# Optimization experiments

Hardware: AMD Instinct MI355X
Metric: run time of the kernel (lower is better)

Reference implementation:

```python
import jax, jax.numpy as jnp
import numpy as np

N, L, V, D, E, NL = 50000, 32, 5000, 128, 800000, 3
P, B = 5000, 64

def setup_inputs() -> dict:
    key = jax.random.key(0)
    ks = jax.random.split(key, 6)
    x = jax.random.randint(ks[0], (N, L), 0, V)            # token ids, 0 = pad
    edge_index = jax.random.randint(ks[1], (2, E), 0, N)   # [2,E] src,dst
    pool_idx = jnp.arange(N) // (N // P)                   # node -> pooled supernode
    node_batch = pool_idx * B // P                         # node -> graph id (grouped, as in torch loop)
    embed = jax.random.normal(ks[2], (V, D), jnp.float32) * 0.02
    W_l = jax.random.normal(ks[3], (NL, D, D), jnp.float32) / np.sqrt(D)
    W_r = jax.random.normal(ks[4], (NL, D, D), jnp.float32) / np.sqrt(D)
    b = jnp.zeros((NL, D), jnp.float32)
    return dict(x=x, edge_index=edge_index, pool_idx=pool_idx, node_batch=node_batch,
                num_pooled=P, embed=embed, W_l=W_l, W_r=W_r, b=b)

def reference(x, edge_index, pool_idx, node_batch, num_pooled, embed, W_l, W_r, b):
    n = x.shape[0]
    dt = embed.dtype
    # masked mean-pool of token embeddings (pad id = 0), length clamped to >=1
    mask = (x != 0)
    lengths = jnp.clip(mask.sum(axis=1), 1, None).astype(dt)          # [N]
    h = (embed[x] * mask[..., None].astype(dt)).sum(axis=1) / lengths[:, None]  # [N,D]
    src, dst = edge_index[0], edge_index[1]
    deg = jnp.clip(jax.ops.segment_sum(jnp.ones(src.shape[0], dt), dst, num_segments=n), 1.0, None)
    # SAGEConv layers: mean-aggregate neighbors, lin_l(agg)+bias + lin_r(self), relu
    # (dropout p=0.5 is identity in eval mode)
    for i in range(W_l.shape[0]):
        agg = jax.ops.segment_sum(h[src], dst, num_segments=n) / deg[:, None]
        h = jax.nn.relu(agg @ W_l[i] + b[i] + h @ W_r[i])
    # global mean pool over supernodes
    cnt = jnp.clip(jax.ops.segment_sum(jnp.ones(n, dt), pool_idx, num_segments=num_pooled), 1.0, None)
    x_pooled = jax.ops.segment_sum(h, pool_idx, num_segments=num_pooled) / cnt[:, None]
    # global max pool of graph ids -> pooled batch vector
    batch_pooled = jax.ops.segment_max(node_batch, pool_idx, num_segments=num_pooled)
    # coalesced pooled edges without self-loops, as a dense boolean adjacency
    sp, dp = pool_idx[src], pool_idx[dst]
    adj = jnp.zeros((num_pooled, num_pooled), jnp.bool_).at[sp, dp].set(True)
    adj = adj & ~jnp.eye(num_pooled, dtype=jnp.bool_)
    return x_pooled, adj, batch_pooled
```

## Files before the change

### kernel.cpp

```cpp
#include <hip/hip_runtime.h>
#include <hip/hip_fp16.h>
#include <limits.h>

#define D 128
#define SCL 64.0f

typedef __attribute__((ext_vector_type(8))) short bf16x8;
typedef __attribute__((ext_vector_type(4))) float f32x4;
typedef __attribute__((ext_vector_type(2))) float f32x2;

#if __has_builtin(__builtin_amdgcn_cvt_pk_f32_fp8) && __has_builtin(__builtin_amdgcn_cvt_pk_fp8_f32)
#define HW_FP8 1
#endif

static __device__ __forceinline__ unsigned short f2bf(float f) {
    unsigned u = __builtin_bit_cast(unsigned, f);
    u += 0x7FFFu + ((u >> 16) & 1u);
    return (unsigned short)(u >> 16);
}
static __device__ __forceinline__ float bf2f(unsigned u16) {
    unsigned u = u16 << 16;
    return __builtin_bit_cast(float, u);
}
static __device__ __forceinline__ bf16x8 load_frag(const unsigned short* p) {
    uint4 v = *(const uint4*)p;
    return __builtin_bit_cast(bf16x8, v);
}
static __device__ __forceinline__ ushort4 pack4(const float* a, float s) {
    ushort4 o;
    o.x = f2bf(a[0] * s); o.y = f2bf(a[1] * s);
    o.z = f2bf(a[2] * s); o.w = f2bf(a[3] * s);
    return o;
}

static __device__ __forceinline__ unsigned char f2q(float v) {
#ifdef HW_FP8
    return (unsigned char)(__builtin_amdgcn_cvt_pk_fp8_f32(v, v, 0, false) & 0xff);
#else
    unsigned short u = __half_as_ushort(__float2half(v));
    u = (unsigned short)(u + 0x7F + ((u >> 8) & 1));
    return (unsigned char)(u >> 8);
#endif
}
static __device__ __forceinline__ unsigned enc4(float a0, float a1, float a2, float a3) {
#ifdef HW_FP8
    unsigned u = __builtin_amdgcn_cvt_pk_fp8_f32(a0, a1, 0, false);
    u = __builtin_amdgcn_cvt_pk_fp8_f32(a2, a3, (int)u, true);
    return u;
#else
    return (unsigned)f2q(a0) | ((unsigned)f2q(a1) << 8) |
           ((unsigned)f2q(a2) << 16) | ((unsigned)f2q(a3) << 24);
#endif
}
static __device__ __forceinline__ void dec4(float* a, unsigned u) {
#ifdef HW_FP8
    f32x2 lo = __builtin_amdgcn_cvt_pk_f32_fp8((int)u, false);
    f32x2 hi = __builtin_amdgcn_cvt_pk_f32_fp8((int)u, true);
    a[0] += lo.x; a[1] += lo.y; a[2] += hi.x; a[3] += hi.y;
#else
    a[0] += __half2float(__ushort_as_half((unsigned short)((u & 0xff) << 8)));
    a[1] += __half2float(__ushort_as_half((unsigned short)(((u >> 8) & 0xff) << 8)));
    a[2] += __half2float(__ushort_as_half((unsigned short)(((u >> 16) & 0xff) << 8)));
    a[3] += __half2float(__ushort_as_half((unsigned short)((u >> 24) << 8)));
#endif
}

__global__ __launch_bounds__(256) void zero_k(float4* __restrict__ b, size_t nb)
{
    size_t i = (size_t)blockIdx.x * 256 + threadIdx.x;
    if (i < nb) b[i] = make_float4(0.f, 0.f, 0.f, 0.f);
}

__global__ __launch_bounds__(256) void epack_k(
    const float* __restrict__ embed, unsigned* __restrict__ e8, int n4)
{
    int i = blockIdx.x * 256 + threadIdx.x;
    if (i >= n4) return;
    float4 v = *(const float4*)&embed[(size_t)i * 4];
    e8[i] = enc4(v.x * SCL, v.y * SCL, v.z * SCL, v.w * SCL);
}

__global__ __launch_bounds__(256) void wpack_k(
    const float* __restrict__ Wl, const float* __restrict__ Wr,
    unsigned short* __restrict__ Wp, int NL)
{
    int idx = blockIdx.x * 256 + threadIdx.x;
    if (idx >= NL * 2 * 16384) return;
    int m = idx >> 14;
    int r = idx & 16383;
    int j = r & 7;
    int lane = (r >> 3) & 63;
    int cb = (r >> 9) & 7;
    int kb = (r >> 12) & 3;
    const float* W = ((m & 1) ? Wr : Wl) + (size_t)(m >> 1) * D * D;
    int k = kb * 32 + (lane >> 4) * 8 + j;
    int c = cb * 16 + (lane & 15);
    Wp[idx] = f2bf(W[(size_t)k * D + c]);
}

__global__ __launch_bounds__(256) void embed_pool_k(
    const int* __restrict__ x, const unsigned char* __restrict__ e8,
    unsigned short* __restrict__ h16, unsigned char* __restrict__ h8, int n, int L)
{
    __shared__ int toks[16][32];
    int t = threadIdx.x;
    int sub = t >> 4, s = t & 15;
    int node = blockIdx.x * 16 + sub;
    for (int j = t; j < 16 * L; j += 256) {
        int nd = blockIdx.x * 16 + j / L;
        toks[j / L][j % L] = (nd < n) ? x[(size_t)nd * L + (j % L)] : 0;
    }
    __syncthreads();
    if (node >= n) return;
    float acc[8] = {};
    int cnt = 0;
    for (int l = 0; l < L; ++l) {
        int tok = toks[sub][l];
        if (tok != 0) {
            uint2 v = *(const uint2*)&e8[(size_t)tok * D + s * 8];
            dec4(acc, v.x); dec4(acc + 4, v.y);
            cnt++;
        }
    }
    float c = (float)(cnt > 0 ? cnt : 1);
    float invh = 1.0f / (SCL * c);
    float inv8 = 1.0f / c;
    ushort4 lo = pack4(acc, invh), hi = pack4(acc + 4, invh);
    *(ushort4*)&h16[(size_t)node * D + s * 8]     = lo;
    *(ushort4*)&h16[(size_t)node * D + s * 8 + 4] = hi;
    uint2 q;
    q.x = enc4(acc[0] * inv8, acc[1] * inv8, acc[2] * inv8, acc[3] * inv8);
    q.y = enc4(acc[4] * inv8, acc[5] * inv8, acc[6] * inv8, acc[7] * inv8);
    *(uint2*)&h8[(size_t)node * D + s * 8] = q;
}

__global__ __launch_bounds__(256) void deg_k(
    const int* __restrict__ ei, int* __restrict__ deg, int E)
{
    int e = blockIdx.x * 256 + threadIdx.x;
    if (e >= E) return;
    atomicAdd(&deg[ei[E + e]], 1);
}

__global__ __launch_bounds__(256) void scan_partial_k(
    const int* __restrict__ deg, int* __restrict__ bsum, int n)
{
    int b = blockIdx.x, t = threadIdx.x;
    int i0 = b * 1024 + t * 4;
    int s = 0;
    #pragma unroll
    for (int k = 0; k < 4; ++k) { int i = i0 + k; if (i < n) s += deg[i]; }
    for (int off = 32; off > 0; off >>= 1) s += __shfl_down(s, off, 64);
    __shared__ int sm4[4];
    if ((t & 63) == 0) sm4[t >> 6] = s;
    __syncthreads();
    if (t == 0) bsum[b] = sm4[0] + sm4[1] + sm4[2] + sm4[3];
}

__global__ __launch_bounds__(256) void scan_bsum_k(
    const int* __restrict__ bsum, int* __restrict__ boff, int nb)
{
    __shared__ int sm[256];
    int t = threadIdx.x;
    sm[t] = (t < nb) ? bsum[t] : 0;
    __syncthreads();
    for (int off = 1; off < 256; off <<= 1) {
        int add = (t >= off) ? sm[t - off] : 0;
        __syncthreads();
        sm[t] += add;
        __syncthreads();
    }
    if (t < nb) boff[t] = (t > 0) ? sm[t - 1] : 0;
}

__global__ __launch_bounds__(256) void scan_final_k(
    const int* __restrict__ deg, const int* __restrict__ boff,
    int* __restrict__ rp, int n)
{
    __shared__ int sm[256];
    int b = blockIdx.x, t = threadIdx.x;
    int i0 = b * 1024 + t * 4;
    int v[4];
    #pragma unroll
    for (int k = 0; k < 4; ++k) { int i = i0 + k; v[k] = (i < n) ? deg[i] : 0; }
    v[1] += v[0]; v[2] += v[1]; v[3] += v[2];
    sm[t] = v[3];
    __syncthreads();
    for (int off = 1; off < 256; off <<= 1) {
        int add = (t >= off) ? sm[t - off] : 0;
        __syncthreads();
        sm[t] += add;
        __syncthreads();
    }
    int base = boff[b] + ((t > 0) ? sm[t - 1] : 0);
    if (b == 0 && t == 0) rp[0] = 0;
    #pragma unroll
    for (int k = 0; k < 4; ++k) {
        int i = i0 + k;
        if (i < n) rp[i + 1] = base + v[k];
    }
}

__global__ __launch_bounds__(256) void edge_pass2_k(
    const int* __restrict__ ei, const int* __restrict__ rp,
    const int* __restrict__ pool, int* __restrict__ cur,
    int* __restrict__ col, float* __restrict__ adj, int E, int P)
{
    int e = blockIdx.x * 256 + threadIdx.x;
    if (e >= E) return;
    int src = ei[e], dst = ei[E + e];
    int pos = atomicAdd(&cur[dst], 1);
    col[rp[dst] + pos] = src;
    int sp = pool[src], dp = pool[dst];
    if (sp != dp) adj[(size_t)sp * P + dp] = 1.0f;
}

__global__ __launch_bounds__(256) void aggregate_k(
    const unsigned char* __restrict__ h8, const int* __restrict__ rp,
    const int* __restrict__ col, unsigned short* __restrict__ agg16, int n)
{
    int node = blockIdx.x * 4 + (threadIdx.x >> 6);
    int lane = threadIdx.x & 63;
    if (node >= n) return;
    int beg = rp[node], end = rp[node + 1];
    int q = lane >> 4, s = lane & 15;
    float acc[8] = {};
    int e = beg + q;
    for (; e + 4 < end; e += 8) {
        int c0 = col[e], c1 = col[e + 4];
        uint2 v0 = *(const uint2*)&h8[(size_t)c0 * D + s * 8];
        uint2 v1 = *(const uint2*)&h8[(size_t)c1 * D + s * 8];
        dec4(acc, v0.x); dec4(acc + 4, v0.y);
        dec4(acc, v1.x); dec4(acc + 4, v1.y);
    }
    if (e < end) {
        uint2 v0 = *(const uint2*)&h8[(size_t)col[e] * D + s * 8];
        dec4(acc, v0.x); dec4(acc + 4, v0.y);
    }
    #pragma unroll
    for (int k = 0; k < 8; ++k) {
        acc[k] += __shfl_xor(acc[k], 16, 64);
        acc[k] += __shfl_xor(acc[k], 32, 64);
    }
    if (q == 0) {
        int dg = end - beg;
        float inv = 1.0f / (SCL * (float)(dg > 0 ? dg : 1));
        ushort4 lo = pack4(acc, inv), hi = pack4(acc + 4, inv);
        *(ushort4*)&agg16[(size_t)node * D + s * 8]     = lo;
        *(ushort4*)&agg16[(size_t)node * D + s * 8 + 4] = hi;
    }
}

__global__ __launch_bounds__(256) void sage_gemm_mfma_k(
    const unsigned short* __restrict__ agg16, unsigned short* __restrict__ h16,
    unsigned char* __restrict__ h8, const unsigned short* __restrict__ Wp,
    const float* __restrict__ bias, int n, int write8)
{
    int t = threadIdx.x;
    int w = t >> 6, lane = t & 63;
    int node0 = blockIdx.x * 128 + w * 32;
    int row = lane & 15, g = lane >> 4;

    f32x4 acc[2][8];
    #pragma unroll
    for (int i = 0; i < 2; ++i)
        #pragma unroll
        for (int c = 0; c < 8; ++c)
            acc[i][c] = (f32x4){0.f, 0.f, 0.f, 0.f};

    float bs[8];
    #pragma unroll
    for (int cb = 0; cb < 8; ++cb) bs[cb] = bias[cb * 16 + row];

    bool ok0 = (node0 < n);
    bool ok1 = (node0 + 16 < n);

    #pragma unroll
    for (int kb = 0; kb < 8; ++kb) {
        const unsigned short* Asrc = (kb < 4) ? agg16 : h16;
        int ko = (kb & 3) * 32 + g * 8;
        bf16x8 a0 = (bf16x8){0,0,0,0,0,0,0,0};
        bf16x8 a1 = a0;
        if (ok0) a0 = load_frag(&Asrc[(size_t)(node0 + row) * D + ko]);
        if (ok1) a1 = load_frag(&Asrc[(size_t)(node0 + 16 + row) * D + ko]);
        const unsigned short* wp = Wp + ((kb < 4) ? 0 : 16384) + (size_t)(kb & 3) * 4096;
        #pragma unroll
        for (int cb = 0; cb < 8; ++cb) {
            bf16x8 b = load_frag(&wp[(cb * 64 + lane) * 8]);
            acc[0][cb] = __builtin_amdgcn_mfma_f32_16x16x32_bf16(a0, b, acc[0][cb], 0, 0, 0);
            acc[1][cb] = __builtin_amdgcn_mfma_f32_16x16x32_bf16(a1, b, acc[1][cb], 0, 0, 0);
        }
    }

    #pragma unroll
    for (int rg = 0; rg < 2; ++rg) {
        int nb = node0 + rg * 16;
        if (nb >= n) break;
        #pragma unroll
        for (int cb = 0; cb < 8; ++cb) {
            int c = cb * 16 + row;
            #pragma unroll
            for (int j = 0; j < 4; ++j) {
                int node = nb + g * 4 + j;
                float v = fmaxf(acc[rg][cb][j] + bs[cb], 0.f);
                h16[(size_t)node * D + c] = f2bf(v);
                if (write8) h8[(size_t)node * D + c] = f2q(v * SCL);
            }
        }
    }
}

__global__ __launch_bounds__(128) void poolmean_k(
    const unsigned short* __restrict__ h16, const int* __restrict__ pool,
    const int* __restrict__ nbatch, float* __restrict__ outx,
    float* __restrict__ outb, int n, int P)
{
    int p = blockIdx.x;
    int d = threadIdx.x;
    int lo = 0, hi = n;
    while (lo < hi) { int mid = (lo + hi) >> 1; if (pool[mid] < p) lo = mid + 1; else hi = mid; }
    int s = lo;
    hi = n;
    while (lo < hi) { int mid = (lo + hi) >> 1; if (pool[mid] < p + 1) lo = mid + 1; else hi = mid; }
    int e = lo;
    float s0 = 0.f, s1 = 0.f, s2 = 0.f, s3 = 0.f;
    int i = s;
    for (; i + 3 < e; i += 4) {
        s0 += bf2f(h16[(size_t)(i + 0) * D + d]);
        s1 += bf2f(h16[(size_t)(i + 1) * D + d]);
        s2 += bf2f(h16[(size_t)(i + 2) * D + d]);
        s3 += bf2f(h16[(size_t)(i + 3) * D + d]);
    }
    for (; i < e; ++i) s0 += bf2f(h16[(size_t)i * D + d]);
    float sum = (s0 + s1) + (s2 + s3);
    int c = e - s;
    outx[(size_t)p * D + d] = sum / (float)(c > 0 ? c : 1);
    if (d == 0) {
        int bm = INT_MIN;
        for (int j = s; j < e; ++j) bm = max(bm, nbatch[j]);
        outb[p] = (float)bm;
    }
}

extern "C" void kernel_launch(void* const* d_in, const int* in_sizes, int n_in,
                              void* d_out, int out_size, void* d_ws, size_t ws_size,
                              hipStream_t stream)
{
    const int*   x      = (const int*)d_in[0];
    const int*   ei     = (const int*)d_in[1];
    const int*   pool   = (const int*)d_in[2];
    const int*   nbatch = (const int*)d_in[3];
    const float* embed  = (const float*)d_in[5];
    const float* Wl     = (const float*)d_in[6];
    const float* Wr     = (const float*)d_in[7];
    const float* bias   = (const float*)d_in[8];

    const int N  = in_sizes[2];
    const int L  = in_sizes[0] / N;
    const int E  = in_sizes[1] / 2;
    const int VD = in_sizes[5];
    const int NL = in_sizes[6] / (D * D);
    const int P  = 5000;

    float* out_x   = (float*)d_out;
    float* out_adj = out_x + (size_t)P * D;
    float* out_b   = out_adj + (size_t)P * P;

    char* w = (char*)d_ws;
    auto alloc = [&](size_t bytes) { void* p = w; w += (bytes + 255) & ~255ULL; return p; };
    size_t ND = (size_t)N * D;
    unsigned short* h16   = (unsigned short*)alloc(ND * 2);
    unsigned short* agg16 = (unsigned short*)alloc(ND * 2);
    unsigned char*  h8    = (unsigned char*)alloc(ND);
    unsigned short* Wp    = (unsigned short*)alloc((size_t)NL * 2 * 16384 * 2);
    unsigned char*  e8    = (unsigned char*)alloc((size_t)VD);
    int*   col  = (int*)alloc((size_t)E * 4);
    int*   rp   = (int*)alloc((size_t)(N + 1) * 4);
    int*   bsum = (int*)alloc(256 * 4);
    int*   boff = (int*)alloc(256 * 4);
    int*   deg  = (int*)alloc((size_t)N * 2 * 4);
    int*   cur  = deg + N;

    const int NB = (N + 1023) / 1024;

    size_t nb = (size_t)N * 2 / 4;
    zero_k<<<(int)((nb + 255) / 256), 256, 0, stream>>>((float4*)deg, nb);

    epack_k<<<(VD / 4 + 255) / 256, 256, 0, stream>>>(embed, (unsigned*)e8, VD / 4);
    wpack_k<<<(NL * 2 * 16384 + 255) / 256, 256, 0, stream>>>(Wl, Wr, Wp, NL);
    embed_pool_k<<<(N + 15) / 16, 256, 0, stream>>>(x, e8, h16, h8, N, L);
    deg_k<<<(E + 255) / 256, 256, 0, stream>>>(ei, deg, E);
    scan_partial_k<<<NB, 256, 0, stream>>>(deg, bsum, N);
    scan_bsum_k<<<1, 256, 0, stream>>>(bsum, boff, NB);
    scan_final_k<<<NB, 256, 0, stream>>>(deg, boff, rp, N);
    edge_pass2_k<<<(E + 255) / 256, 256, 0, stream>>>(ei, rp, pool, cur, col, out_adj, E, P);

    for (int ly = 0; ly < NL; ++ly) {
        aggregate_k<<<(N + 3) / 4, 256, 0, stream>>>(h8, rp, col, agg16, N);
        sage_gemm_mfma_k<<<(N + 127) / 128, 256, 0, stream>>>(
            agg16, h16, h8, Wp + (size_t)ly * 2 * 16384, bias + (size_t)ly * D, N,
            (ly < NL - 1) ? 1 : 0);
    }

    poolmean_k<<<P, 128, 0, stream>>>(h16, pool, nbatch, out_x, out_b, N, P);
}
```

Baseline: 267.4 us.

## Split int8 node features into two 64-column planes and aggregate each separately

The int8 node-feature buffer is stored as two separate 64-column planes instead of one 128-column array. The embedding and GEMM kernels write into those planes, and neighbour aggregation runs as two passes, one per plane, each filling half of the bf16 aggregate. The aim is to halve the working set of the random neighbour gather so it fits better in the per-XCD L2 and gets fewer misses. The cost is reading the CSR column indices twice per layer, an extra kernel launch per layer, and narrower 4-byte loads per lane.

```diff
diff --git a/kernel.cpp b/kernel.cpp
--- a/kernel.cpp
+++ b/kernel.cpp
@@ -100,7 +100,8 @@
 
 __global__ __launch_bounds__(256) void embed_pool_k(
     const int* __restrict__ x, const unsigned char* __restrict__ e8,
-    unsigned short* __restrict__ h16, unsigned char* __restrict__ h8, int n, int L)
+    unsigned short* __restrict__ h16, unsigned char* __restrict__ h8a,
+    unsigned char* __restrict__ h8b, int n, int L)
 {
     __shared__ int toks[16][32];
     int t = threadIdx.x;
@@ -131,7 +132,9 @@
     uint2 q;
     q.x = enc4(acc[0] * inv8, acc[1] * inv8, acc[2] * inv8, acc[3] * inv8);
     q.y = enc4(acc[4] * inv8, acc[5] * inv8, acc[6] * inv8, acc[7] * inv8);
-    *(uint2*)&h8[(size_t)node * D + s * 8] = q;
+    unsigned char* plane = (s < 8) ? h8a : h8b;
+    int so = (s & 7) * 8;
+    *(uint2*)&plane[(size_t)node * 64 + so] = q;
 }
 
 __global__ __launch_bounds__(256) void deg_k(
@@ -216,44 +219,45 @@
 }
 
 __global__ __launch_bounds__(256) void aggregate_k(
-    const unsigned char* __restrict__ h8, const int* __restrict__ rp,
-    const int* __restrict__ col, unsigned short* __restrict__ agg16, int n)
+    const unsigned char* __restrict__ plane, const int* __restrict__ rp,
+    const int* __restrict__ col, unsigned short* __restrict__ agg16,
+    int n, int poff)
 {
     int node = blockIdx.x * 4 + (threadIdx.x >> 6);
     int lane = threadIdx.x & 63;
     if (node >= n) return;
     int beg = rp[node], end = rp[node + 1];
     int q = lane >> 4, s = lane & 15;
-    float acc[8] = {};
+    float acc[4] = {};
     int e = beg + q;
     for (; e + 4 < end; e += 8) {
         int c0 = col[e], c1 = col[e + 4];
-        uint2 v0 = *(const uint2*)&h8[(size_t)c0 * D + s * 8];
-        uint2 v1 = *(const uint2*)&h8[(size_t)c1 * D + s * 8];
-        dec4(acc, v0.x); dec4(acc + 4, v0.y);
-        dec4(acc, v1.x); dec4(acc + 4, v1.y);
+        unsigned v0 = *(const unsigned*)&plane[(size_t)c0 * 64 + s * 4];
+        unsigned v1 = *(const unsigned*)&plane[(size_t)c1 * 64 + s * 4];
+        dec4(acc, v0);
+        dec4(acc, v1);
     }
     if (e < end) {
-        uint2 v0 = *(const uint2*)&h8[(size_t)col[e] * D + s * 8];
-        dec4(acc, v0.x); dec4(acc + 4, v0.y);
-    }
-    #pragma unroll
-    for (int k = 0; k < 8; ++k) {
+        unsigned v0 = *(const unsigned*)&plane[(size_t)col[e] * 64 + s * 4];
+        dec4(acc, v0);
+    }
+    #pragma unroll
+    for (int k = 0; k < 4; ++k) {
         acc[k] += __shfl_xor(acc[k], 16, 64);
         acc[k] += __shfl_xor(acc[k], 32, 64);
     }
     if (q == 0) {
         int dg = end - beg;
         float inv = 1.0f / (SCL * (float)(dg > 0 ? dg : 1));
-        ushort4 lo = pack4(acc, inv), hi = pack4(acc + 4, inv);
-        *(ushort4*)&agg16[(size_t)node * D + s * 8]     = lo;
-        *(ushort4*)&agg16[(size_t)node * D + s * 8 + 4] = hi;
+        ushort4 o = pack4(acc, inv);
+        *(ushort4*)&agg16[(size_t)node * D + poff + s * 4] = o;
     }
 }
 
 __global__ __launch_bounds__(256) void sage_gemm_mfma_k(
     const unsigned short* __restrict__ agg16, unsigned short* __restrict__ h16,
-    unsigned char* __restrict__ h8, const unsigned short* __restrict__ Wp,
+    unsigned char* __restrict__ h8a, unsigned char* __restrict__ h8b,
+    const unsigned short* __restrict__ Wp,
     const float* __restrict__ bias, int n, int write8)
 {
     int t = threadIdx.x;
@@ -299,12 +303,14 @@
         #pragma unroll
         for (int cb = 0; cb < 8; ++cb) {
             int c = cb * 16 + row;
+            unsigned char* plane = (c < 64) ? h8a : h8b;
+            int co = c & 63;
             #pragma unroll
             for (int j = 0; j < 4; ++j) {
                 int node = nb + g * 4 + j;
                 float v = fmaxf(acc[rg][cb][j] + bs[cb], 0.f);
                 h16[(size_t)node * D + c] = f2bf(v);
-                if (write8) h8[(size_t)node * D + c] = f2q(v * SCL);
+                if (write8) plane[(size_t)node * 64 + co] = f2q(v * SCL);
             }
         }
     }
@@ -371,7 +377,8 @@
     size_t ND = (size_t)N * D;
     unsigned short* h16   = (unsigned short*)alloc(ND * 2);
     unsigned short* agg16 = (unsigned short*)alloc(ND * 2);
-    unsigned char*  h8    = (unsigned char*)alloc(ND);
+    unsigned char*  h8a   = (unsigned char*)alloc(ND / 2);
+    unsigned char*  h8b   = (unsigned char*)alloc(ND / 2);
     unsigned short* Wp    = (unsigned short*)alloc((size_t)NL * 2 * 16384 * 2);
     unsigned char*  e8    = (unsigned char*)alloc((size_t)VD);
     int*   col  = (int*)alloc((size_t)E * 4);
@@ -388,7 +395,7 @@
 
     epack_k<<<(VD / 4 + 255) / 256, 256, 0, stream>>>(embed, (unsigned*)e8, VD / 4);
     wpack_k<<<(NL * 2 * 16384 + 255) / 256, 256, 0, stream>>>(Wl, Wr, Wp, NL);
-    embed_pool_k<<<(N + 15) / 16, 256, 0, stream>>>(x, e8, h16, h8, N, L);
+    embed_pool_k<<<(N + 15) / 16, 256, 0, stream>>>(x, e8, h16, h8a, h8b, N, L);
     deg_k<<<(E + 255) / 256, 256, 0, stream>>>(ei, deg, E);
     scan_partial_k<<<NB, 256, 0, stream>>>(deg, bsum, N);
     scan_bsum_k<<<1, 256, 0, stream>>>(bsum, boff, NB);
@@ -396,9 +403,10 @@
     edge_pass2_k<<<(E + 255) / 256, 256, 0, stream>>>(ei, rp, pool, cur, col, out_adj, E, P);
 
     for (int ly = 0; ly < NL; ++ly) {
-        aggregate_k<<<(N + 3) / 4, 256, 0, stream>>>(h8, rp, col, agg16, N);
+        aggregate_k<<<(N + 3) / 4, 256, 0, stream>>>(h8a, rp, col, agg16, N, 0);
+        aggregate_k<<<(N + 3) / 4, 256, 0, stream>>>(h8b, rp, col, agg16, N, 64);
         sage_gemm_mfma_k<<<(N + 127) / 128, 256, 0, stream>>>(
-            agg16, h16, h8, Wp + (size_t)ly * 2 * 16384, bias + (size_t)ly * D, N,
+            agg16, h16, h8a, h8b, Wp + (size_t)ly * 2 * 16384, bias + (size_t)ly * D, N,
             (ly < NL - 1) ? 1 : 0);
     }
 
```

Result: slower. 319.7 us (+19.5%).
